# Optimization experiments

Measured on AMD Instinct MI355X. Metric: run time of the kernel, lower is better.

## Reference

```python
import jax, jax.numpy as jnp
import numpy as np

B, M, N, I, O, NM = 16, 256, 256, 64, 64, 16


def setup_inputs() -> dict:
    key = jax.random.key(0)
    k1, k2, k3, k4, k5 = jax.random.split(key, 5)
    glorot = 1.0 / np.sqrt(I + O)
    return {
        "x": jax.random.normal(k1, (B, M, N, I), dtype=jnp.float32),
        "fw1": jax.random.normal(k2, (I, O, NM, NM, 2), dtype=jnp.float32) * glorot,
        "fw2": jax.random.normal(k3, (I, O, NM, NM, 2), dtype=jnp.float32) * glorot,
        "W": jax.random.normal(k4, (I, O), dtype=jnp.float32) * glorot,
        "b": jnp.zeros((O,), dtype=jnp.float32),
    }


def reference(x, fw1, fw2, W, b):
    # x: [B, M, N, I] -> [B, I, M, N]
    Bs, Ms, Ns, Is = x.shape
    nm = fw1.shape[2]
    xt = jnp.transpose(x, (0, 3, 1, 2))
    # forward rFFT over spatial dims, scaled by 1/sqrt(M*N) as in the TF code
    x_ft = jnp.fft.rfft2(xt, s=(Ms, Ns))  # [B, I, M, N//2+1] complex64
    x_ft = x_ft / jnp.asarray(np.sqrt(Ms * Ns), dtype=x_ft.dtype)
    # complex weights (stack-of-2 real/imag -> complex); complex einsum is
    # exactly the real/imag stacked matmul in the original
    w1 = jax.lax.complex(fw1[..., 0], fw1[..., 1])
    w2 = jax.lax.complex(fw2[..., 0], fw2[..., 1])
    top = jnp.einsum('bixy,ioxy->boxy', x_ft[:, :, :nm, :nm], w1)
    bot = jnp.einsum('bixy,ioxy->boxy', x_ft[:, :, -nm:, :nm], w2)
    mid = jnp.zeros((Bs, top.shape[1], Ms - 2 * nm, nm), dtype=top.dtype)
    out_ft = jnp.concatenate([top, mid, bot], axis=2)          # [B, O, M, nm]
    pad = jnp.zeros((Bs, top.shape[1], Ms, Ms // 2 + 1 - nm), dtype=top.dtype)
    out_ft = jnp.concatenate([out_ft, pad], axis=3)            # [B, O, M, M//2+1]
    y = jnp.fft.irfft2(out_ft, s=(Ns, Ms))                     # [B, O, N, M]
    # TF rescale: sqrt(prod of last two dims of out_ft) = sqrt(N*(M//2+1))
    y = y * jnp.asarray(np.sqrt(Ns * (Ms // 2 + 1)), dtype=y.dtype)
    y = jnp.transpose(y, (0, 2, 3, 1))                         # [B, M, N, O]
    return jax.nn.relu(y @ W + b + y)
```

## Files before the change

### kernel.cpp

```cpp
#include <hip/hip_runtime.h>
#include <hip/hip_bf16.h>


#define PI2F 6.283185307179586f

typedef __attribute__((ext_vector_type(8))) short short8v;
typedef __attribute__((ext_vector_type(4))) float f32x4;

static __device__ __forceinline__ unsigned short f_to_bf16(float f) {
  unsigned int u = __float_as_uint(f);
  u += 0x7fffu + ((u >> 16) & 1u);
  return (unsigned short)(u >> 16);
}
static __device__ __forceinline__ unsigned int pack_bf16(float lo, float hi) {
  return (unsigned int)f_to_bf16(lo) | ((unsigned int)f_to_bf16(hi) << 16);
}

__global__ __launch_bounds__(256) void k_prep(const float* __restrict__ fw1,
                                              const float* __restrict__ fw2,
                                              float2* __restrict__ wT,
                                              unsigned short* __restrict__ Eg,
                                              unsigned short* __restrict__ CSg,
                                              const float* __restrict__ Wg,
                                              unsigned short* __restrict__ Wtb) {
  int t = threadIdx.x;
  if (blockIdx.x == 256) {
    const float SC = 1.0f / 256.0f;
#pragma unroll
    for (int ky = 0; ky < 16; ++ky) {
      int idx = (ky * t) & 255;
      float ss, cc;
      sincosf(PI2F * (float)idx * (1.0f / 256.0f), &ss, &cc);
      Eg[(2 * ky) * 256 + t]     = f_to_bf16(cc * SC);
      Eg[(2 * ky + 1) * 256 + t] = f_to_bf16(-ss * SC);
      CSg[t * 32 + 2 * ky]       = f_to_bf16(cc);
      CSg[t * 32 + 2 * ky + 1]   = f_to_bf16(ss);
    }
#pragma unroll
    for (int k = 0; k < 16; ++k) {
      int p = k * 256 + t;
      Wtb[(p & 63) * 64 + (p >> 6)] = f_to_bf16(Wg[p]);
    }
    return;
  }
  int a  = blockIdx.x >> 3;
  int ic = blockIdx.x & 7;
  const float* w = (a < 16) ? fw1 : fw2;
  int xx = a & 15;
#pragma unroll
  for (int k = 0; k < 2; ++k) {
    int p = k * 256 + t;
    int i = ic * 8 + (p >> 6);
    int o = p & 63;
    const float4* s4 = reinterpret_cast<const float4*>(
        w + ((((size_t)i * 64 + o) * 16 + xx) * 16) * 2);
#pragma unroll
    for (int j = 0; j < 8; ++j) {
      float4 q = s4[j];
      wT[(((size_t)(2 * j) * 32 + a) * 64 + i) * 64 + o]     = make_float2(q.x, q.y);
      wT[(((size_t)(2 * j + 1) * 32 + a) * 64 + i) * 64 + o] = make_float2(q.z, q.w);
    }
  }
}

__global__ __launch_bounds__(256) void k1_mfma(const float* __restrict__ x,
                                               const unsigned short* __restrict__ Eg,
                                               unsigned int* __restrict__ Tb) {
  __shared__ __align__(16) unsigned short El[32 * 264];
  __shared__ __align__(16) float xs[2][2048];
  int bm = blockIdx.x;
  int b = bm >> 8, m = bm & 255;
  int tid = threadIdx.x;

  {
    const unsigned int* src = reinterpret_cast<const unsigned int*>(Eg);
    unsigned int* dst = reinterpret_cast<unsigned int*>(El);
#pragma unroll
    for (int t = 0; t < 16; ++t) {
      int idx = t * 256 + tid;
      dst[(idx >> 7) * 132 + (idx & 127)] = src[idx];
    }
  }

  const float* xrow = x + (size_t)bm * 16384;
  int lane = tid & 63, w = tid >> 6;
  int r16 = lane & 15, g4 = lane >> 4;

  int r0 = tid >> 4;
  int c4 = (tid & 15) * 4;
  int off0 = r0 * 64 + (c4 ^ (((r0 >> 3) & 3) << 4));
  int r1 = 16 + r0;
  int off1 = r1 * 64 + (c4 ^ (((r1 >> 3) & 3) << 4));
  int colr = (w * 16 + r16) ^ (g4 << 4);

  {
    const float4* s = reinterpret_cast<const float4*>(xrow);
    float4 v0 = s[tid], v1 = s[256 + tid];
    *reinterpret_cast<float4*>(&xs[0][off0]) = v0;
    *reinterpret_cast<float4*>(&xs[0][off1]) = v1;
  }
  __syncthreads();

  f32x4 z = {0.f, 0.f, 0.f, 0.f};
  f32x4 acc0 = z, acc1 = z;

#pragma unroll
  for (int c = 0; c < 8; ++c) {
    int cur = c & 1;
    if (c < 7) {
      const float4* s = reinterpret_cast<const float4*>(xrow + (c + 1) * 2048);
      float4 v0 = s[tid], v1 = s[256 + tid];
      *reinterpret_cast<float4*>(&xs[cur ^ 1][off0]) = v0;
      *reinterpret_cast<float4*>(&xs[cur ^ 1][off1]) = v1;
    }
    const float* xb = &xs[cur][g4 * 8 * 64 + colr];
    float xv[8];
#pragma unroll
    for (int j = 0; j < 8; ++j) xv[j] = xb[j * 64];
    short8v bfr;
#pragma unroll
    for (int j = 0; j < 8; ++j) bfr[j] = (short)f_to_bf16(xv[j]);
    int nb = c * 32 + g4 * 8;
    short8v a0 = *reinterpret_cast<const short8v*>(&El[r16 * 264 + nb]);
    short8v a1 = *reinterpret_cast<const short8v*>(&El[(16 + r16) * 264 + nb]);
    acc0 = __builtin_amdgcn_mfma_f32_16x16x32_bf16(a0, bfr, acc0, 0, 0, 0);
    acc1 = __builtin_amdgcn_mfma_f32_16x16x32_bf16(a1, bfr, acc1, 0, 0, 0);
    __syncthreads();
  }

  int i = w * 16 + r16;
#pragma unroll
  for (int mt = 0; mt < 2; ++mt) {
    f32x4 av = (mt == 0) ? acc0 : acc1;
    int ky_a = mt * 8 + g4 * 2;
    Tb[((size_t)(b * 16 + ky_a) * 256 + m) * 64 + i]     = pack_bf16(av[0], av[1]);
    Tb[((size_t)(b * 16 + ky_a + 1) * 256 + m) * 64 + i] = pack_bf16(av[2], av[3]);
  }
}

__global__ __launch_bounds__(256) void k2_fwd_m(const unsigned int* __restrict__ Tb,
                                                float* __restrict__ Xp) {
  int bx = blockIdx.x;
  int bky = bx & 255, mc = bx >> 8;
  int m0 = mc * 64;
  int ih = threadIdx.x & 15;
  int ag = threadIdx.x >> 4;
  const uint4* Tp4 = reinterpret_cast<const uint4*>(Tb) + (size_t)bky * 4096 + ih;

  float cd1, sd1n, cd2, sd2n;
  { float ss, cc; sincosf(PI2F * (float)ag * (1.0f / 256.0f), &ss, &cc); cd1 = cc; sd1n = -ss; }
  { float ss, cc; sincosf(PI2F * (float)(ag - 16) * (1.0f / 256.0f), &ss, &cc); cd2 = cc; sd2n = -ss; }
  float c1, s1, c2, s2;
  { int t = (ag * m0) & 255; float ss, cc; sincosf(PI2F * (float)t * (1.0f / 256.0f), &ss, &cc); c1 = cc; s1 = -ss; }
  { int t = ((ag + 240) * m0) & 255; float ss, cc; sincosf(PI2F * (float)t * (1.0f / 256.0f), &ss, &cc); c2 = cc; s2 = -ss; }

  float xr1[4], xi1[4], xr2[4], xi2[4];
#pragma unroll
  for (int ii = 0; ii < 4; ++ii) { xr1[ii] = xi1[ii] = xr2[ii] = xi2[ii] = 0.0f; }

#pragma unroll 4
  for (int m = 0; m < 64; ++m) {
    uint4 q = Tp4[(size_t)(m0 + m) * 16];
    unsigned int dv[4] = {q.x, q.y, q.z, q.w};
    float tre[4], tim[4];
#pragma unroll
    for (int ii = 0; ii < 4; ++ii) {
      tre[ii] = __uint_as_float(dv[ii] << 16);
      tim[ii] = __uint_as_float(dv[ii] & 0xffff0000u);
    }
#pragma unroll
    for (int ii = 0; ii < 4; ++ii) {
      xr1[ii] += tre[ii] * c1 - tim[ii] * s1;
      xi1[ii] += tre[ii] * s1 + tim[ii] * c1;
      xr2[ii] += tre[ii] * c2 - tim[ii] * s2;
      xi2[ii] += tre[ii] * s2 + tim[ii] * c2;
    }
    float cn;
    cn = c1 * cd1 - s1 * sd1n; s1 = c1 * sd1n + s1 * cd1; c1 = cn;
    cn = c2 * cd2 - s2 * sd2n; s2 = c2 * sd2n + s2 * cd2; c2 = cn;
  }

  float* Xb = Xp + (size_t)mc * 1048576;
  float* Xp1 = Xb + ((size_t)bky * 32 + ag) * 128 + ih * 8;
  float* Xp2 = Xb + ((size_t)bky * 32 + ag + 16) * 128 + ih * 8;
  reinterpret_cast<float4*>(Xp1)[0] = make_float4(xr1[0], xi1[0], xr1[1], xi1[1]);
  reinterpret_cast<float4*>(Xp1)[1] = make_float4(xr1[2], xi1[2], xr1[3], xi1[3]);
  reinterpret_cast<float4*>(Xp2)[0] = make_float4(xr2[0], xi2[0], xr2[1], xi2[1]);
  reinterpret_cast<float4*>(Xp2)[1] = make_float4(xr2[2], xi2[2], xr2[3], xi2[3]);
}

__global__ __launch_bounds__(256) void k3_mix(const float* __restrict__ Xp,
                                              const float* __restrict__ wT,
                                              float* __restrict__ OF) {
  int blk = blockIdx.x;
  int kyy = blk >> 5, a = blk & 31;
  __shared__ float wre[64 * 65];
  __shared__ float wim[64 * 65];
  __shared__ float xsh[16 * 128];

  const float2* wsrc = reinterpret_cast<const float2*>(wT) + (size_t)(kyy * 32 + a) * 4096;
#pragma unroll
  for (int k = 0; k < 16; ++k) {
    int p = k * 256 + (int)threadIdx.x;
    float2 v = wsrc[p];
    int i = p >> 6, o = p & 63;
    wre[i * 65 + o] = v.x;
    wim[i * 65 + o] = v.y;
  }
  {
    int bb = threadIdx.x >> 4, icn = threadIdx.x & 15;
    size_t off = ((size_t)(bb * 16 + kyy) * 32 + a) * 128;
    float4 a0 = make_float4(0.f, 0.f, 0.f, 0.f), a1 = a0;
#pragma unroll
    for (int c = 0; c < 4; ++c) {
      const float4* xsrc = reinterpret_cast<const float4*>(Xp + (size_t)c * 1048576 + off);
      float4 q0 = xsrc[icn * 2], q1 = xsrc[icn * 2 + 1];
      a0.x += q0.x; a0.y += q0.y; a0.z += q0.z; a0.w += q0.w;
      a1.x += q1.x; a1.y += q1.y; a1.z += q1.z; a1.w += q1.w;
    }
    float4* xdst = reinterpret_cast<float4*>(xsh + bb * 128);
    xdst[icn * 2]     = a0;
    xdst[icn * 2 + 1] = a1;
  }
  __syncthreads();

  int o = threadIdx.x & 63, bg = threadIdx.x >> 6;
#pragma unroll
  for (int bb = 0; bb < 4; ++bb) {
    int b = bg * 4 + bb;
    float ore = 0.0f, oim = 0.0f;
    for (int i = 0; i < 64; ++i) {
      float xr = xsh[b * 128 + 2 * i], xi = xsh[b * 128 + 2 * i + 1];
      float wr = wre[i * 65 + o],     wi = wim[i * 65 + o];
      ore += xr * wr - xi * wi;
      oim += xr * wi + xi * wr;
    }
    reinterpret_cast<float2*>(OF)[(((size_t)b * 16 + kyy) * 32 + a) * 64 + o] =
        make_float2(ore, oim);
  }
}

__global__ __launch_bounds__(256) void k4_inv_kx(const float* __restrict__ OF,
                                                 uint4* __restrict__ Gb4) {
  int bx = blockIdx.x;
  int b = bx >> 6, ug = (bx >> 2) & 15, chunk = bx & 3;
  __shared__ float ct[256], st[256];
  {
    float ssv, ccv;
    sincosf(PI2F * (float)threadIdx.x * (1.0f / 256.0f), &ssv, &ccv);
    ct[threadIdx.x] = ccv;
    st[threadIdx.x] = ssv;
  }
  __syncthreads();

  int o = threadIdx.x & 63, us = threadIdx.x >> 6;
  int u0 = ug * 16 + us * 4;
  const float SC2 = 0.002772904280510622f;
  const float2* OFb = reinterpret_cast<const float2*>(OF) +
                      ((size_t)b * 16 + chunk * 4) * 2048;

  float accr[4][4], acci[4][4];
#pragma unroll
  for (int du = 0; du < 4; ++du)
#pragma unroll
    for (int kyl = 0; kyl < 4; ++kyl) { accr[du][kyl] = 0.0f; acci[du][kyl] = 0.0f; }

  for (int a = 0; a < 32; ++a) {
    int kx = (a < 16) ? a : (224 + a);
    float ofr[4], ofi[4];
#pragma unroll
    for (int kyl = 0; kyl < 4; ++kyl) {
      float2 v = OFb[(kyl * 32 + a) * 64 + o];
      ofr[kyl] = v.x; ofi[kyl] = v.y;
    }
#pragma unroll
    for (int du = 0; du < 4; ++du) {
      int t = (kx * (u0 + du)) & 255;
      float cv = ct[t], sv = st[t];
#pragma unroll
      for (int kyl = 0; kyl < 4; ++kyl) {
        accr[du][kyl] += ofr[kyl] * cv - ofi[kyl] * sv;
        acci[du][kyl] += ofr[kyl] * sv + ofi[kyl] * cv;
      }
    }
  }
#pragma unroll
  for (int du = 0; du < 4; ++du) {
    int u = u0 + du;
    unsigned int wv[4];
#pragma unroll
    for (int kyl = 0; kyl < 4; ++kyl) {
      int ky = chunk * 4 + kyl;
      float sc = SC2 * ((ky == 0) ? 1.0f : 2.0f);
      wv[kyl] = pack_bf16(accr[du][kyl] * sc, -acci[du][kyl] * sc);
    }
    uint4 pk; pk.x = wv[0]; pk.y = wv[1]; pk.z = wv[2]; pk.w = wv[3];
    Gb4[(((size_t)b * 256 + u) * 4 + chunk) * 64 + o] = pk;
  }
}

__global__ __launch_bounds__(256) void k5_mfma(const unsigned short* __restrict__ Gb,
                                               const unsigned short* __restrict__ CSg,
                                               const unsigned short* __restrict__ Wtb,
                                               const float* __restrict__ bias,
                                               float* __restrict__ out) {
  __shared__ __align__(16) unsigned short yl[256 * 72];

  int blk = blockIdx.x;
  int tid = threadIdx.x;
  int lane = tid & 63, w = tid >> 6;
  int r16 = lane & 15, g4 = lane >> 4;
  int kc0 = g4 * 8;

  f32x4 z = {0.f, 0.f, 0.f, 0.f};
  f32x4 acc[4][4];

  short8v af[4], bfx[4];
#pragma unroll
  for (int vt = 0; vt < 4; ++vt)
    af[vt] = *reinterpret_cast<const short8v*>(&CSg[(w * 64 + vt * 16 + r16) * 32 + kc0]);
#pragma unroll
  for (int ot = 0; ot < 4; ++ot)
    bfx[ot] = *reinterpret_cast<const short8v*>(
        &Gb[(((size_t)blk * 4 + g4) * 64 + ot * 16 + r16) * 8]);
#pragma unroll
  for (int vt = 0; vt < 4; ++vt)
#pragma unroll
    for (int ot = 0; ot < 4; ++ot)
      acc[vt][ot] = __builtin_amdgcn_mfma_f32_16x16x32_bf16(af[vt], bfx[ot], z, 0, 0, 0);

#pragma unroll
  for (int vt = 0; vt < 4; ++vt)
#pragma unroll
    for (int ot = 0; ot < 4; ++ot)
#pragma unroll
      for (int r = 0; r < 4; ++r)
        yl[(w * 64 + vt * 16 + g4 * 4 + r) * 72 + ot * 16 + r16] = f_to_bf16(acc[vt][ot][r]);

#pragma unroll
  for (int ot = 0; ot < 4; ++ot) {
    float bv = bias[ot * 16 + r16];
#pragma unroll
    for (int vt = 0; vt < 4; ++vt)
#pragma unroll
      for (int r = 0; r < 4; ++r) acc[vt][ot][r] += bv;
  }

#pragma unroll
  for (int ks = 0; ks < 2; ++ks) {
    int k0 = ks * 32 + kc0;
    short8v ya[4], wb[4];
#pragma unroll
    for (int vt = 0; vt < 4; ++vt)
      ya[vt] = *reinterpret_cast<const short8v*>(&yl[(w * 64 + vt * 16 + r16) * 72 + k0]);
#pragma unroll
    for (int ot = 0; ot < 4; ++ot)
      wb[ot] = *reinterpret_cast<const short8v*>(&Wtb[(ot * 16 + r16) * 64 + k0]);
#pragma unroll
    for (int vt = 0; vt < 4; ++vt)
#pragma unroll
      for (int ot = 0; ot < 4; ++ot)
        acc[vt][ot] = __builtin_amdgcn_mfma_f32_16x16x32_bf16(ya[vt], wb[ot], acc[vt][ot], 0, 0, 0);
  }

  float* ob = out + (size_t)blk * 16384;
  float* tw = reinterpret_cast<float*>(&yl[w * 4608]);
#pragma unroll
  for (int vt = 0; vt < 4; ++vt) {
#pragma unroll
    for (int ot = 0; ot < 4; ++ot)
#pragma unroll
      for (int r = 0; r < 4; ++r)
        tw[(g4 * 4 + r) * 68 + ot * 16 + r16] = fmaxf(acc[vt][ot][r], 0.0f);
    float* obase = ob + (size_t)(w * 64 + vt * 16) * 64;
#pragma unroll
    for (int q = 0; q < 4; ++q) {
      float4 vv = *reinterpret_cast<const float4*>(
          &tw[(q * 4 + (lane >> 4)) * 68 + (lane & 15) * 4]);
      *reinterpret_cast<float4*>(&obase[q * 256 + lane * 4]) = vv;
    }
  }
}

extern "C" void kernel_launch(void* const* d_in, const int* in_sizes, int n_in,
                              void* d_out, int out_size, void* d_ws, size_t ws_size,
                              hipStream_t stream) {
  const float* x   = (const float*)d_in[0];
  const float* fw1 = (const float*)d_in[1];
  const float* fw2 = (const float*)d_in[2];
  const float* W   = (const float*)d_in[3];
  const float* bb  = (const float*)d_in[4];
  float* out = (float*)d_out;

  float* ws = (float*)d_ws;
  float* wT          = ws;
  unsigned int* Tb   = (unsigned int*)(ws + 4194304);
  float* Xp          = ws + 8388608;
  float* OF          = ws + 12582912;
  unsigned int* Gb   = (unsigned int*)(ws + 13631488);
  unsigned short* Eg  = (unsigned short*)(ws + 17825792);
  unsigned short* CSg = Eg + 8192;
  unsigned short* Wtb = CSg + 8192;

  hipLaunchKernelGGL(k_prep,   dim3(257),  dim3(256), 0, stream,
                     fw1, fw2, (float2*)wT, Eg, CSg, W, Wtb);
  hipLaunchKernelGGL(k1_mfma,  dim3(4096), dim3(256), 0, stream, x, Eg, Tb);
  hipLaunchKernelGGL(k2_fwd_m, dim3(1024), dim3(256), 0, stream, Tb, Xp);
  hipLaunchKernelGGL(k3_mix,   dim3(512),  dim3(256), 0, stream, Xp, wT, OF);
  hipLaunchKernelGGL(k4_inv_kx,dim3(1024), dim3(256), 0, stream, OF, (uint4*)Gb);
  hipLaunchKernelGGL(k5_mfma,  dim3(4096), dim3(256), 0, stream,
                     (const unsigned short*)Gb, CSg, Wtb, bb, out);
}
```

Measured before the change: 234.6 us.

## Fuse forward M-DFT with spectral mixing and store mode weights as bf16

The forward DFT along M (k2) and the complex channel mixing (k3) now run as one kernel with 1024 threads per (b,ky) block. The four M-chunk partial sums are reduced in shared memory, so the Xp round-trip through global memory is gone. The spectral weights are packed as bf16 real/imag pairs, which halves weight traffic, and are read straight from global memory rather than staged in LDS. The risks are that the grid shrinks to 256 large blocks, each weight tensor is now re-read by 16 blocks (one per batch), and bf16 weights lose precision.

```diff
diff --git a/kernel.cpp b/kernel.cpp
--- a/kernel.cpp
+++ b/kernel.cpp
@@ -18,7 +18,7 @@
 
 __global__ __launch_bounds__(256) void k_prep(const float* __restrict__ fw1,
                                               const float* __restrict__ fw2,
-                                              float2* __restrict__ wT,
+                                              unsigned int* __restrict__ wTb,
                                               unsigned short* __restrict__ Eg,
                                               unsigned short* __restrict__ CSg,
                                               const float* __restrict__ Wg,
@@ -57,8 +57,8 @@
 #pragma unroll
     for (int j = 0; j < 8; ++j) {
       float4 q = s4[j];
-      wT[(((size_t)(2 * j) * 32 + a) * 64 + i) * 64 + o]     = make_float2(q.x, q.y);
-      wT[(((size_t)(2 * j + 1) * 32 + a) * 64 + i) * 64 + o] = make_float2(q.z, q.w);
+      wTb[(((size_t)(2 * j) * 32 + a) * 64 + i) * 64 + o]     = pack_bf16(q.x, q.y);
+      wTb[(((size_t)(2 * j + 1) * 32 + a) * 64 + i) * 64 + o] = pack_bf16(q.z, q.w);
     }
   }
 }
@@ -138,13 +138,17 @@
   }
 }
 
-__global__ __launch_bounds__(256) void k2_fwd_m(const unsigned int* __restrict__ Tb,
-                                                float* __restrict__ Xp) {
-  int bx = blockIdx.x;
-  int bky = bx & 255, mc = bx >> 8;
+__global__ __launch_bounds__(1024) void k23_mix(const unsigned int* __restrict__ Tb,
+                                                const unsigned int* __restrict__ wTb,
+                                                float* __restrict__ OF) {
+  __shared__ float Xpr[4][2048];
+  __shared__ float Xpi[4][2048];
+  int bky = blockIdx.x;
+  int ky = bky & 15;
+  int tid = threadIdx.x;
+
+  int mc = tid >> 8, ih = tid & 15, ag = (tid >> 4) & 15;
   int m0 = mc * 64;
-  int ih = threadIdx.x & 15;
-  int ag = threadIdx.x >> 4;
   const uint4* Tp4 = reinterpret_cast<const uint4*>(Tb) + (size_t)bky * 4096 + ih;
 
   float cd1, sd1n, cd2, sd2n;
@@ -179,63 +183,39 @@
     cn = c1 * cd1 - s1 * sd1n; s1 = c1 * sd1n + s1 * cd1; c1 = cn;
     cn = c2 * cd2 - s2 * sd2n; s2 = c2 * sd2n + s2 * cd2; c2 = cn;
   }
-
-  float* Xb = Xp + (size_t)mc * 1048576;
-  float* Xp1 = Xb + ((size_t)bky * 32 + ag) * 128 + ih * 8;
-  float* Xp2 = Xb + ((size_t)bky * 32 + ag + 16) * 128 + ih * 8;
-  reinterpret_cast<float4*>(Xp1)[0] = make_float4(xr1[0], xi1[0], xr1[1], xi1[1]);
-  reinterpret_cast<float4*>(Xp1)[1] = make_float4(xr1[2], xi1[2], xr1[3], xi1[3]);
-  reinterpret_cast<float4*>(Xp2)[0] = make_float4(xr2[0], xi2[0], xr2[1], xi2[1]);
-  reinterpret_cast<float4*>(Xp2)[1] = make_float4(xr2[2], xi2[2], xr2[3], xi2[3]);
-}
-
-__global__ __launch_bounds__(256) void k3_mix(const float* __restrict__ Xp,
-                                              const float* __restrict__ wT,
-                                              float* __restrict__ OF) {
-  int blk = blockIdx.x;
-  int kyy = blk >> 5, a = blk & 31;
-  __shared__ float wre[64 * 65];
-  __shared__ float wim[64 * 65];
-  __shared__ float xsh[16 * 128];
-
-  const float2* wsrc = reinterpret_cast<const float2*>(wT) + (size_t)(kyy * 32 + a) * 4096;
-#pragma unroll
-  for (int k = 0; k < 16; ++k) {
-    int p = k * 256 + (int)threadIdx.x;
-    float2 v = wsrc[p];
-    int i = p >> 6, o = p & 63;
-    wre[i * 65 + o] = v.x;
-    wim[i * 65 + o] = v.y;
-  }
-  {
-    int bb = threadIdx.x >> 4, icn = threadIdx.x & 15;
-    size_t off = ((size_t)(bb * 16 + kyy) * 32 + a) * 128;
-    float4 a0 = make_float4(0.f, 0.f, 0.f, 0.f), a1 = a0;
-#pragma unroll
-    for (int c = 0; c < 4; ++c) {
-      const float4* xsrc = reinterpret_cast<const float4*>(Xp + (size_t)c * 1048576 + off);
-      float4 q0 = xsrc[icn * 2], q1 = xsrc[icn * 2 + 1];
-      a0.x += q0.x; a0.y += q0.y; a0.z += q0.z; a0.w += q0.w;
-      a1.x += q1.x; a1.y += q1.y; a1.z += q1.z; a1.w += q1.w;
-    }
-    float4* xdst = reinterpret_cast<float4*>(xsh + bb * 128);
-    xdst[icn * 2]     = a0;
-    xdst[icn * 2 + 1] = a1;
+#pragma unroll
+  for (int ii = 0; ii < 4; ++ii) {
+    Xpr[mc][ag * 64 + ih * 4 + ii]        = xr1[ii];
+    Xpi[mc][ag * 64 + ih * 4 + ii]        = xi1[ii];
+    Xpr[mc][(ag + 16) * 64 + ih * 4 + ii] = xr2[ii];
+    Xpi[mc][(ag + 16) * 64 + ih * 4 + ii] = xi2[ii];
   }
   __syncthreads();
 
-  int o = threadIdx.x & 63, bg = threadIdx.x >> 6;
-#pragma unroll
-  for (int bb = 0; bb < 4; ++bb) {
-    int b = bg * 4 + bb;
+#pragma unroll
+  for (int j = 0; j < 2; ++j) {
+    int s = j * 1024 + tid;
+    Xpr[0][s] += Xpr[1][s] + Xpr[2][s] + Xpr[3][s];
+    Xpi[0][s] += Xpi[1][s] + Xpi[2][s] + Xpi[3][s];
+  }
+  __syncthreads();
+
+  int o = tid & 63, ab = tid >> 6;
+#pragma unroll
+  for (int half = 0; half < 2; ++half) {
+    int a = ab + half * 16;
+    const unsigned int* wp = wTb + (size_t)(ky * 32 + a) * 4096 + o;
     float ore = 0.0f, oim = 0.0f;
     for (int i = 0; i < 64; ++i) {
-      float xr = xsh[b * 128 + 2 * i], xi = xsh[b * 128 + 2 * i + 1];
-      float wr = wre[i * 65 + o],     wi = wim[i * 65 + o];
+      float xr = Xpr[0][a * 64 + i];
+      float xi = Xpi[0][a * 64 + i];
+      unsigned int wv = wp[i * 64];
+      float wr = __uint_as_float(wv << 16);
+      float wi = __uint_as_float(wv & 0xffff0000u);
       ore += xr * wr - xi * wi;
       oim += xr * wi + xi * wr;
     }
-    reinterpret_cast<float2*>(OF)[(((size_t)b * 16 + kyy) * 32 + a) * 64 + o] =
+    reinterpret_cast<float2*>(OF)[((size_t)bky * 32 + a) * 64 + o] =
         make_float2(ore, oim);
   }
 }
@@ -393,21 +373,19 @@
   float* out = (float*)d_out;
 
   float* ws = (float*)d_ws;
-  float* wT          = ws;
-  unsigned int* Tb   = (unsigned int*)(ws + 4194304);
-  float* Xp          = ws + 8388608;
-  float* OF          = ws + 12582912;
-  unsigned int* Gb   = (unsigned int*)(ws + 13631488);
-  unsigned short* Eg  = (unsigned short*)(ws + 17825792);
+  unsigned int* wTb  = (unsigned int*)ws;
+  unsigned int* Tb   = (unsigned int*)(ws + 2097152);
+  float* OF          = ws + 6291456;
+  unsigned int* Gb   = (unsigned int*)(ws + 7340032);
+  unsigned short* Eg  = (unsigned short*)(ws + 11534336);
   unsigned short* CSg = Eg + 8192;
   unsigned short* Wtb = CSg + 8192;
 
-  hipLaunchKernelGGL(k_prep,   dim3(257),  dim3(256), 0, stream,
-                     fw1, fw2, (float2*)wT, Eg, CSg, W, Wtb);
-  hipLaunchKernelGGL(k1_mfma,  dim3(4096), dim3(256), 0, stream, x, Eg, Tb);
-  hipLaunchKernelGGL(k2_fwd_m, dim3(1024), dim3(256), 0, stream, Tb, Xp);
-  hipLaunchKernelGGL(k3_mix,   dim3(512),  dim3(256), 0, stream, Xp, wT, OF);
-  hipLaunchKernelGGL(k4_inv_kx,dim3(1024), dim3(256), 0, stream, OF, (uint4*)Gb);
-  hipLaunchKernelGGL(k5_mfma,  dim3(4096), dim3(256), 0, stream,
+  hipLaunchKernelGGL(k_prep,   dim3(257),  dim3(256),  0, stream,
+                     fw1, fw2, wTb, Eg, CSg, W, Wtb);
+  hipLaunchKernelGGL(k1_mfma,  dim3(4096), dim3(256),  0, stream, x, Eg, Tb);
+  hipLaunchKernelGGL(k23_mix,  dim3(256),  dim3(1024), 0, stream, Tb, wTb, OF);
+  hipLaunchKernelGGL(k4_inv_kx,dim3(1024), dim3(256),  0, stream, OF, (uint4*)Gb);
+  hipLaunchKernelGGL(k5_mfma,  dim3(4096), dim3(256),  0, stream,
                      (const unsigned short*)Gb, CSg, Wtb, bb, out);
 }
```

Result: faster. 209.9 us, median of 2 (-10.5%).
